# Performance work log

Hardware: AMD Instinct MI355X
Metric: run time of the kernel (lower is better)

## Reference

```python
import jax, jax.numpy as jnp
import numpy as np

N = 10000   # nodes
E = 80000   # edges per graph (avg degree 8)
H = 32      # hidden width (hard-coded in module)
VD0 = 2048  # visual_dim for gcn_0
VD1 = 256   # visual_dim // 8 for gcn_b21


def setup_inputs() -> dict:
    key = jax.random.key(0)
    ks = jax.random.split(key, 16)
    rn = lambda k, s, sc=1.0: jax.random.normal(k, s, dtype=jnp.float32) * sc
    return {
        "x": rn(ks[0], (N, 9)),
        "vis0": rn(ks[1], (N, VD0)),
        "vis1": rn(ks[2], (N, VD1)),
        "edge_index0": jax.random.randint(ks[3], (2, E), 0, N),
        "edge_index1": jax.random.randint(ks[4], (2, E), 0, N),
        # input_mlp: Linear(9,32) -> BatchNorm1d(32) (eval) -> PReLU -> Dropout(0) -> Linear(32,32)
        "W_in1": rn(ks[5], (9, H), 0.3), "b_in1": jnp.zeros((H,), jnp.float32),
        "bn_gamma": jnp.ones((H,), jnp.float32), "bn_beta": jnp.zeros((H,), jnp.float32),
        "bn_mean": jnp.zeros((H,), jnp.float32), "bn_var": jnp.ones((H,), jnp.float32),
        "prelu_a": jnp.asarray(0.25, jnp.float32),
        "W_in2": rn(ks[6], (H, H), 0.15), "b_in2": jnp.zeros((H,), jnp.float32),
        "w_node": rn(ks[7], (H, 1), 0.15), "b_node": jnp.zeros((1,), jnp.float32),
        "W_c0": rn(ks[8], (H, H), 0.15), "b_c0": jnp.zeros((H,), jnp.float32),
        "W_c1": rn(ks[9], (H, H), 0.15), "b_c1": jnp.zeros((H,), jnp.float32),
        "w_p0": rn(ks[10], (H, 1), 0.15), "b_p0": jnp.zeros((1,), jnp.float32),
        "w_p1": rn(ks[11], (H, 1), 0.15), "b_p1": jnp.zeros((1,), jnp.float32),
    }


def _cm_cos_conv(h, edge_index, vis, W, b):
    # gather-weight-scatter: w_e = cos(vis[src], vis[dst]); out_i = (sum_e->i w_e * h[src_e]) @ W + b
    src, dst = edge_index[0], edge_index[1]
    vn = vis * jax.lax.rsqrt(jnp.sum(vis * vis, axis=-1, keepdims=True) + 1e-8)
    w = jnp.sum(vn[src] * vn[dst], axis=-1)  # [E] cosine similarity per edge
    agg = jax.ops.segment_sum(h[src] * w[:, None], dst, num_segments=h.shape[0])  # [N,H]
    return agg @ W + b  # conv_activation=None -> identity


def reference(x, vis0, vis1, edge_index0, edge_index1, W_in1, b_in1, bn_gamma, bn_beta, bn_mean, bn_var, prelu_a, W_in2, b_in2, w_node, b_node, W_c0, b_c0, W_c1, b_c1, w_p0, b_p0, w_p1, b_p1):
    h = x @ W_in1 + b_in1
    h = bn_gamma * (h - bn_mean) * jax.lax.rsqrt(bn_var + 1e-5) + bn_beta
    h = jnp.where(h >= 0, h, prelu_a * h)  # PReLU (single shared slope)
    h = h @ W_in2 + b_in2                   # [N,32] shared for graphs 0 and 4
    nodes_scores = (h @ w_node + b_node)[:, 0]
    h0 = _cm_cos_conv(h, edge_index0, vis0, W_c0, b_c0)
    h1 = _cm_cos_conv(h, edge_index1, vis1, W_c1, b_c1)
    s0 = (h0 @ w_p0 + b_p0)[:, 0]
    s1 = (h1 @ w_p1 + b_p1)[:, 0]
    return nodes_scores + s0 + s1
```

## Files before the change

kernel.cpp:

```cpp
#include <hip/hip_runtime.h>

#define N_NODES 10000
#define NE      80000
#define H       32
#define VD0     2048
#define VD1     256

#define EDGE_CAP 32

#define NODE_BLOCKS  40
#define NC_BLOCKS    2500
#define PREP_BLOCKS  (NODE_BLOCKS + 2 * NC_BLOCKS)

#define EDGE0_PHASES  4
#define EDGE0_GBLK    2500
#define EDGE0_BLOCKS  (EDGE0_PHASES * EDGE0_GBLK)
#define EDGE1_BLOCKS  2500
#define EDGE_BLOCKS   (EDGE0_BLOCKS + EDGE1_BLOCKS)

__device__ inline unsigned short f2bf_rne(float f) {
    unsigned int u = __float_as_uint(f);
    u += 0x7fffu + ((u >> 16) & 1u);
    return (unsigned short)(u >> 16);
}
__device__ inline float bflo(unsigned int u) { return __uint_as_float(u << 16); }
__device__ inline float bfhi(unsigned int u) { return __uint_as_float(u & 0xffff0000u); }
__device__ inline float bfs(unsigned short u) { return __uint_as_float((unsigned int)u << 16); }

__device__ inline float dot8_bf16(uint4 a, uint4 b) {
    float s;
    s  = bflo(a.x) * bflo(b.x) + bfhi(a.x) * bfhi(b.x);
    s += bflo(a.y) * bflo(b.y) + bfhi(a.y) * bfhi(b.y);
    s += bflo(a.z) * bflo(b.z) + bfhi(a.z) * bfhi(b.z);
    s += bflo(a.w) * bflo(b.w) + bfhi(a.w) * bfhi(b.w);
    return s;
}
__device__ inline float dot4_bf16(uint2 a, uint2 b) {
    return bflo(a.x) * bflo(b.x) + bfhi(a.x) * bfhi(b.x)
         + bflo(a.y) * bflo(b.y) + bfhi(a.y) * bfhi(b.y);
}

template <int VD>
__device__ inline void normconv_node(const float* __restrict__ vis,
                                     unsigned short* __restrict__ vn,
                                     int node, int lane)
{
    const float4* v = (const float4*)(vis + (size_t)node * VD);
    float4 f[VD / 256];
    float acc = 0.f;
    #pragma unroll
    for (int it = 0; it < VD / 256; it++) {
        f[it] = v[it * 64 + lane];
        acc += f[it].x * f[it].x + f[it].y * f[it].y + f[it].z * f[it].z + f[it].w * f[it].w;
    }
    #pragma unroll
    for (int o = 32; o; o >>= 1) acc += __shfl_xor(acc, o);
    const float inv = rsqrtf(acc + 1e-8f);
    ushort4* o4 = (ushort4*)(vn + (size_t)node * VD);
    #pragma unroll
    for (int it = 0; it < VD / 256; it++) {
        ushort4 r;
        r.x = f2bf_rne(f[it].x * inv);
        r.y = f2bf_rne(f[it].y * inv);
        r.z = f2bf_rne(f[it].z * inv);
        r.w = f2bf_rne(f[it].w * inv);
        o4[it * 64 + lane] = r;
    }
}

__global__ __launch_bounds__(256) void prep_kernel(
    const float* __restrict__ x,
    const float* __restrict__ vis0, const float* __restrict__ vis1,
    const float* __restrict__ W_in1, const float* __restrict__ b_in1,
    const float* __restrict__ bn_gamma, const float* __restrict__ bn_beta,
    const float* __restrict__ bn_mean, const float* __restrict__ bn_var,
    const float* __restrict__ prelu_a,
    const float* __restrict__ W_in2, const float* __restrict__ b_in2,
    const float* __restrict__ w_node, const float* __restrict__ b_node,
    const float* __restrict__ W_c0, const float* __restrict__ b_c0,
    const float* __restrict__ W_c1, const float* __restrict__ b_c1,
    const float* __restrict__ w_p0, const float* __restrict__ b_p0,
    const float* __restrict__ w_p1, const float* __restrict__ b_p1,
    float* __restrict__ out, float* __restrict__ p0w, float* __restrict__ p1w,
    unsigned short* __restrict__ vn0, unsigned short* __restrict__ vn1)
{
    const int bid = blockIdx.x;
    const int t   = threadIdx.x;

    if (bid < NODE_BLOCKS) {
        __shared__ float sW1[9 * H];
        __shared__ float sW2[H * H];
        __shared__ float sU0[H], sU1[H], sWn[H];
        __shared__ float sB1[H], sB2[H], sSc[H], sSh[H];
        __shared__ float sC;

        for (int i = t; i < 9 * H; i += 256) sW1[i] = W_in1[i];
        for (int i = t; i < H * H; i += 256) sW2[i] = W_in2[i];
        if (t < H) {
            sB1[t] = b_in1[t];
            sB2[t] = b_in2[t];
            float sc = bn_gamma[t] * rsqrtf(bn_var[t] + 1e-5f);
            sSc[t] = sc;
            sSh[t] = bn_beta[t] - bn_mean[t] * sc;
            sWn[t] = w_node[t];
            float u0 = 0.f, u1 = 0.f;
            for (int j = 0; j < H; j++) {
                u0 += W_c0[t * H + j] * w_p0[j];
                u1 += W_c1[t * H + j] * w_p1[j];
            }
            sU0[t] = u0; sU1[t] = u1;
        }
        if (t == 0) {
            float c0 = b_p0[0], c1 = b_p1[0];
            for (int j = 0; j < H; j++) { c0 += b_c0[j] * w_p0[j]; c1 += b_c1[j] * w_p1[j]; }
            sC = c0 + c1 + b_node[0];
        }
        __syncthreads();

        const float a = prelu_a[0];
        const int n = bid * 256 + t;
        if (n >= N_NODES) return;

        float xi[9];
        #pragma unroll
        for (int i = 0; i < 9; i++) xi[i] = x[n * 9 + i];

        float tt[H];
        #pragma unroll
        for (int j = 0; j < H; j++) {
            float s = sB1[j];
            #pragma unroll
            for (int i = 0; i < 9; i++) s += xi[i] * sW1[i * H + j];
            s = s * sSc[j] + sSh[j];
            tt[j] = s >= 0.f ? s : a * s;
        }

        float ns = 0.f, p0 = 0.f, p1 = 0.f;
        #pragma unroll
        for (int k = 0; k < H; k++) {
            float h = sB2[k];
            #pragma unroll
            for (int j = 0; j < H; j++) h += tt[j] * sW2[j * H + k];
            ns += h * sWn[k];
            p0 += h * sU0[k];
            p1 += h * sU1[k];
        }
        out[n] = ns + sC;
        p0w[n] = p0;
        p1w[n] = p1;
    } else if (bid < NODE_BLOCKS + NC_BLOCKS) {
        const int node = ((bid - NODE_BLOCKS) * 256 + t) >> 6;
        if (node < N_NODES) normconv_node<VD0>(vis0, vn0, node, t & 63);
    } else {
        const int node = ((bid - NODE_BLOCKS - NC_BLOCKS) * 256 + t) >> 6;
        if (node < N_NODES) normconv_node<VD1>(vis1, vn1, node, t & 63);
    }
}

__global__ __launch_bounds__(256) void scatter_kernel(
    const int* __restrict__ ei0, int* __restrict__ cur0, uint2* __restrict__ b0,
    const float* __restrict__ p0w, const unsigned short* __restrict__ vn0,
    const int* __restrict__ ei1, int* __restrict__ cur1, uint2* __restrict__ b1,
    const float* __restrict__ p1w, const unsigned short* __restrict__ vn1,
    float* __restrict__ out)
{
    const int e = blockIdx.x * 256 + threadIdx.x;
    if (e >= NE) return;
    {
        const int s = ei0[e];
        const int d = ei0[NE + e];
        const int pos = atomicAdd(&cur0[d], 1);
        if (pos < EDGE_CAP) {
            b0[d * EDGE_CAP + pos] = make_uint2((unsigned)(s * (VD0 * 2)),
                                                __float_as_uint(p0w[s]));
        } else {
            const unsigned short* a = vn0 + (size_t)s * VD0;
            const unsigned short* c = vn0 + (size_t)d * VD0;
            float acc = 0.f;
            for (int i = 0; i < VD0; i++) acc += bfs(a[i]) * bfs(c[i]);
            atomicAdd(&out[d], acc * p0w[s]);
        }
    }
    {
        const int s = ei1[e];
        const int d = ei1[NE + e];
        const int pos = atomicAdd(&cur1[d], 1);
        if (pos < EDGE_CAP) {
            b1[d * EDGE_CAP + pos] = make_uint2((unsigned)(s * (VD1 * 2)),
                                                __float_as_uint(p1w[s]));
        } else {
            const unsigned short* a = vn1 + (size_t)s * VD1;
            const unsigned short* c = vn1 + (size_t)d * VD1;
            float acc = 0.f;
            for (int i = 0; i < VD1; i++) acc += bfs(a[i]) * bfs(c[i]);
            atomicAdd(&out[d], acc * p1w[s]);
        }
    }
}

__global__ __launch_bounds__(256) void edge_kernel_fused(
    const unsigned short* __restrict__ vn0,
    const uint2* __restrict__ b0, const int* __restrict__ cur0,
    const unsigned short* __restrict__ vn1,
    const uint2* __restrict__ b1, const int* __restrict__ cur1,
    float* __restrict__ out)
{
    const int bid  = blockIdx.x;
    const int lane = threadIdx.x & 63;

    if (bid < EDGE0_BLOCKS) {
        const int phase = bid / EDGE0_GBLK;
        const int group = bid % EDGE0_GBLK;
        const int d     = group * 4 + (threadIdx.x >> 6);
        int cnt = cur0[d];
        if (cnt <= 0) return;
        cnt = cnt < EDGE_CAP ? cnt : EDGE_CAP;
        const int last = cnt - 1;

        const char* base = (const char*)vn0;
        const int koffB  = phase * 1024 + lane * 16;
        const uint4 dreg = *(const uint4*)(base + d * (VD0 * 2) + koffB);
        const uint2* eb  = b0 + d * EDGE_CAP;

        float partial = 0.f;
        for (int j = 0; j < cnt; j += 8) {
            uint2 e[8];
            #pragma unroll
            for (int k = 0; k < 8; k++) {
                int jj = j + k;
                jj = jj > last ? last : jj;
                e[k] = eb[jj];
            }
            uint4 r[8];
            #pragma unroll
            for (int k = 0; k < 8; k++)
                r[k] = *(const uint4*)(base + e[k].x + koffB);
            #pragma unroll
            for (int k = 0; k < 8; k++) {
                const float pw = (j + k <= last) ? __uint_as_float(e[k].y) : 0.f;
                partial += dot8_bf16(dreg, r[k]) * pw;
            }
        }
        #pragma unroll
        for (int o = 32; o; o >>= 1) partial += __shfl_down(partial, o);
        if (lane == 0) atomicAdd(&out[d], partial);
    } else {
        const int d = (bid - EDGE0_BLOCKS) * 4 + (threadIdx.x >> 6);
        int cnt = cur1[d];
        if (cnt <= 0) return;
        cnt = cnt < EDGE_CAP ? cnt : EDGE_CAP;
        const int last = cnt - 1;

        const char* base = (const char*)vn1;
        const int koffB  = lane * 8;
        const uint2 dreg = *(const uint2*)(base + d * (VD1 * 2) + koffB);
        const uint2* eb  = b1 + d * EDGE_CAP;

        float partial = 0.f;
        for (int j = 0; j < cnt; j += 8) {
            uint2 e[8];
            #pragma unroll
            for (int k = 0; k < 8; k++) {
                int jj = j + k;
                jj = jj > last ? last : jj;
                e[k] = eb[jj];
            }
            uint2 r[8];
            #pragma unroll
            for (int k = 0; k < 8; k++)
                r[k] = *(const uint2*)(base + e[k].x + koffB);
            #pragma unroll
            for (int k = 0; k < 8; k++) {
                const float pw = (j + k <= last) ? __uint_as_float(e[k].y) : 0.f;
                partial += dot4_bf16(dreg, r[k]) * pw;
            }
        }
        #pragma unroll
        for (int o = 32; o; o >>= 1) partial += __shfl_down(partial, o);
        if (lane == 0) atomicAdd(&out[d], partial);
    }
}

template <int VD>
__global__ __launch_bounds__(256) void norm_kernel(const float* __restrict__ vis,
                                                   float* __restrict__ inv)
{
    const int wave = (blockIdx.x * 256 + threadIdx.x) >> 6;
    const int lane = threadIdx.x & 63;
    if (wave >= N_NODES) return;
    const float4* v = (const float4*)(vis + (size_t)wave * VD);
    float acc = 0.f;
    #pragma unroll
    for (int it = 0; it < VD / 256; it++) {
        float4 f = v[lane + it * 64];
        acc += f.x * f.x + f.y * f.y + f.z * f.z + f.w * f.w;
    }
    #pragma unroll
    for (int o = 32; o; o >>= 1) acc += __shfl_down(acc, o);
    if (lane == 0) inv[wave] = rsqrtf(acc + 1e-8f);
}

template <int VD>
__global__ __launch_bounds__(256) void edge_kernel(
    const float* __restrict__ vis, const int* __restrict__ ei,
    const float* __restrict__ inv, const float* __restrict__ p,
    float* __restrict__ out)
{
    const int wave = (blockIdx.x * 256 + threadIdx.x) >> 6;
    const int lane = threadIdx.x & 63;
    if (wave >= NE) return;
    const int src = ei[wave];
    const int dst = ei[NE + wave];
    const float4* va = (const float4*)(vis + (size_t)src * VD);
    const float4* vb = (const float4*)(vis + (size_t)dst * VD);
    float acc = 0.f;
    #pragma unroll
    for (int it = 0; it < VD / 256; it++) {
        float4 fa = va[lane + it * 64];
        float4 fb = vb[lane + it * 64];
        acc += fa.x * fb.x + fa.y * fb.y + fa.z * fb.z + fa.w * fb.w;
    }
    #pragma unroll
    for (int o = 32; o; o >>= 1) acc += __shfl_down(acc, o);
    if (lane == 0) {
        float w = acc * inv[src] * inv[dst];
        atomicAdd(&out[dst], w * p[src]);
    }
}

__global__ __launch_bounds__(256) void node_kernel_fb(
    const float* __restrict__ x,
    const float* __restrict__ W_in1, const float* __restrict__ b_in1,
    const float* __restrict__ bn_gamma, const float* __restrict__ bn_beta,
    const float* __restrict__ bn_mean, const float* __restrict__ bn_var,
    const float* __restrict__ prelu_a,
    const float* __restrict__ W_in2, const float* __restrict__ b_in2,
    const float* __restrict__ w_node, const float* __restrict__ b_node,
    const float* __restrict__ W_c0, const float* __restrict__ b_c0,
    const float* __restrict__ W_c1, const float* __restrict__ b_c1,
    const float* __restrict__ w_p0, const float* __restrict__ b_p0,
    const float* __restrict__ w_p1, const float* __restrict__ b_p1,
    float* __restrict__ out, float* __restrict__ p0w, float* __restrict__ p1w)
{
    __shared__ float sW1[9 * H];
    __shared__ float sW2[H * H];
    __shared__ float sU0[H], sU1[H], sWn[H];
    __shared__ float sB1[H], sB2[H], sSc[H], sSh[H];
    __shared__ float sC;

    const int t = threadIdx.x;
    for (int i = t; i < 9 * H; i += 256) sW1[i] = W_in1[i];
    for (int i = t; i < H * H; i += 256) sW2[i] = W_in2[i];
    if (t < H) {
        sB1[t] = b_in1[t];
        sB2[t] = b_in2[t];
        float sc = bn_gamma[t] * rsqrtf(bn_var[t] + 1e-5f);
        sSc[t] = sc;
        sSh[t] = bn_beta[t] - bn_mean[t] * sc;
        sWn[t] = w_node[t];
        float u0 = 0.f, u1 = 0.f;
        for (int j = 0; j < H; j++) {
            u0 += W_c0[t * H + j] * w_p0[j];
            u1 += W_c1[t * H + j] * w_p1[j];
        }
        sU0[t] = u0; sU1[t] = u1;
    }
    if (t == 0) {
        float c0 = b_p0[0], c1 = b_p1[0];
        for (int j = 0; j < H; j++) { c0 += b_c0[j] * w_p0[j]; c1 += b_c1[j] * w_p1[j]; }
        sC = c0 + c1 + b_node[0];
    }
    __syncthreads();

    const float a = prelu_a[0];
    const int n = blockIdx.x * 256 + t;
    if (n >= N_NODES) return;

    float xi[9];
    #pragma unroll
    for (int i = 0; i < 9; i++) xi[i] = x[n * 9 + i];

    float tt[H];
    #pragma unroll
    for (int j = 0; j < H; j++) {
        float s = sB1[j];
        #pragma unroll
        for (int i = 0; i < 9; i++) s += xi[i] * sW1[i * H + j];
        s = s * sSc[j] + sSh[j];
        tt[j] = s >= 0.f ? s : a * s;
    }

    float ns = 0.f, p0 = 0.f, p1 = 0.f;
    #pragma unroll
    for (int k = 0; k < H; k++) {
        float h = sB2[k];
        #pragma unroll
        for (int j = 0; j < H; j++) h += tt[j] * sW2[j * H + k];
        ns += h * sWn[k];
        p0 += h * sU0[k];
        p1 += h * sU1[k];
    }
    out[n] = ns + sC;
    p0w[n] = p0;
    p1w[n] = p1;
}

extern "C" void kernel_launch(void* const* d_in, const int* in_sizes, int n_in,
                              void* d_out, int out_size, void* d_ws, size_t ws_size,
                              hipStream_t stream)
{
    const float* x        = (const float*)d_in[0];
    const float* vis0     = (const float*)d_in[1];
    const float* vis1     = (const float*)d_in[2];
    const int*   ei0      = (const int*)d_in[3];
    const int*   ei1      = (const int*)d_in[4];
    const float* W_in1    = (const float*)d_in[5];
    const float* b_in1    = (const float*)d_in[6];
    const float* bn_gamma = (const float*)d_in[7];
    const float* bn_beta  = (const float*)d_in[8];
    const float* bn_mean  = (const float*)d_in[9];
    const float* bn_var   = (const float*)d_in[10];
    const float* prelu_a  = (const float*)d_in[11];
    const float* W_in2    = (const float*)d_in[12];
    const float* b_in2    = (const float*)d_in[13];
    const float* w_node   = (const float*)d_in[14];
    const float* b_node   = (const float*)d_in[15];
    const float* W_c0     = (const float*)d_in[16];
    const float* b_c0     = (const float*)d_in[17];
    const float* W_c1     = (const float*)d_in[18];
    const float* b_c1     = (const float*)d_in[19];
    const float* w_p0     = (const float*)d_in[20];
    const float* b_p0     = (const float*)d_in[21];
    const float* w_p1     = (const float*)d_in[22];
    const float* b_p1     = (const float*)d_in[23];

    float* out = (float*)d_out;

    char* ws = (char*)d_ws;
    float* p0w  = (float*)ws;                  ws += N_NODES * 4;
    float* p1w  = (float*)ws;                  ws += N_NODES * 4;
    float* inv0 = (float*)ws;                  ws += N_NODES * 4;
    float* inv1 = (float*)ws;                  ws += N_NODES * 4;
    unsigned short* vn0 = (unsigned short*)ws; ws += (size_t)N_NODES * VD0 * 2;
    unsigned short* vn1 = (unsigned short*)ws; ws += (size_t)N_NODES * VD1 * 2;
    uint2* b0   = (uint2*)ws;                  ws += (size_t)N_NODES * EDGE_CAP * 8;
    uint2* b1   = (uint2*)ws;                  ws += (size_t)N_NODES * EDGE_CAP * 8;
    int* cur0   = (int*)ws;                    ws += N_NODES * 4;
    int* cur1   = (int*)ws;                    ws += N_NODES * 4;
    const size_t need = (size_t)(ws - (char*)d_ws);

    if (ws_size >= need) {
        hipMemsetAsync(cur0, 0, 2 * N_NODES * sizeof(int), stream);

        prep_kernel<<<PREP_BLOCKS, 256, 0, stream>>>(
            x, vis0, vis1,
            W_in1, b_in1, bn_gamma, bn_beta, bn_mean, bn_var, prelu_a,
            W_in2, b_in2, w_node, b_node, W_c0, b_c0, W_c1, b_c1,
            w_p0, b_p0, w_p1, b_p1,
            out, p0w, p1w, vn0, vn1);

        scatter_kernel<<<(NE + 255) / 256, 256, 0, stream>>>(
            ei0, cur0, b0, p0w, vn0,
            ei1, cur1, b1, p1w, vn1, out);

        edge_kernel_fused<<<EDGE_BLOCKS, 256, 0, stream>>>(
            vn0, b0, cur0, vn1, b1, cur1, out);
    } else {
        node_kernel_fb<<<(N_NODES + 255) / 256, 256, 0, stream>>>(
            x, W_in1, b_in1, bn_gamma, bn_beta, bn_mean, bn_var, prelu_a,
            W_in2, b_in2, w_node, b_node, W_c0, b_c0, W_c1, b_c1,
            w_p0, b_p0, w_p1, b_p1, out, p0w, p1w);
        norm_kernel<VD0><<<(N_NODES * 64 + 255) / 256, 256, 0, stream>>>(vis0, inv0);
        norm_kernel<VD1><<<(N_NODES * 64 + 255) / 256, 256, 0, stream>>>(vis1, inv1);
        edge_kernel<VD0><<<(NE * 64 + 255) / 256, 256, 0, stream>>>(vis0, ei0, inv0, p0w, out);
        edge_kernel<VD1><<<(NE * 64 + 255) / 256, 256, 0, stream>>>(vis1, ei1, inv1, p1w, out);
    }
}
```

Before: 238.8 us.

## Fuse prep, scatter and edge stages into one cooperative persistent kernel

Replaces the memset plus three separate kernel launches with a single cooperative persistent kernel. It zeroes the counters in-kernel, then runs the node MLP and normalisation stage, the edge bucketing stage and the per-destination dot stage, separated by grid-wide syncs. The goal is to remove launch gaps and kernel tails. The graph-0 edge stage also splits into 8 phases of 4 bf16 elements instead of 4 phases of 8, which changes per-lane load width and parallelism. Grid syncs and a grid capped at 4096 blocks with forced occupancy of 4 may leave stages under-parallelised, and the per-call static occupancy query adds host logic.

```diff
diff --git a/kernel.cpp b/kernel.cpp
--- a/kernel.cpp
+++ b/kernel.cpp
@@ -1,4 +1,7 @@
 #include <hip/hip_runtime.h>
+#include <hip/hip_cooperative_groups.h>
+
+namespace cg = cooperative_groups;
 
 #define N_NODES 10000
 #define NE      80000
@@ -8,15 +11,15 @@
 
 #define EDGE_CAP 32
 
-#define NODE_BLOCKS  40
-#define NC_BLOCKS    2500
-#define PREP_BLOCKS  (NODE_BLOCKS + 2 * NC_BLOCKS)
-
-#define EDGE0_PHASES  4
-#define EDGE0_GBLK    2500
-#define EDGE0_BLOCKS  (EDGE0_PHASES * EDGE0_GBLK)
-#define EDGE1_BLOCKS  2500
-#define EDGE_BLOCKS   (EDGE0_BLOCKS + EDGE1_BLOCKS)
+#define A_MLP    40
+#define A_NC0    2500
+#define A_NC1    2500
+#define A_UNITS  (A_MLP + A_NC0 + A_NC1)
+#define ZERO_BLOCKS 79
+
+#define C_PHASES 8
+#define C_G0     (C_PHASES * 2500)
+#define C_UNITS  (C_G0 + 2500)
 
 __device__ inline unsigned short f2bf_rne(float f) {
     unsigned int u = __float_as_uint(f);
@@ -27,18 +30,30 @@
 __device__ inline float bfhi(unsigned int u) { return __uint_as_float(u & 0xffff0000u); }
 __device__ inline float bfs(unsigned short u) { return __uint_as_float((unsigned int)u << 16); }
 
-__device__ inline float dot8_bf16(uint4 a, uint4 b) {
-    float s;
-    s  = bflo(a.x) * bflo(b.x) + bfhi(a.x) * bfhi(b.x);
-    s += bflo(a.y) * bflo(b.y) + bfhi(a.y) * bfhi(b.y);
-    s += bflo(a.z) * bflo(b.z) + bfhi(a.z) * bfhi(b.z);
-    s += bflo(a.w) * bflo(b.w) + bfhi(a.w) * bfhi(b.w);
-    return s;
-}
 __device__ inline float dot4_bf16(uint2 a, uint2 b) {
     return bflo(a.x) * bflo(b.x) + bfhi(a.x) * bfhi(b.x)
          + bflo(a.y) * bflo(b.y) + bfhi(a.y) * bfhi(b.y);
 }
+
+struct KP {
+    const float* x;
+    const float* vis0; const float* vis1;
+    const int* ei0; const int* ei1;
+    const float* W_in1; const float* b_in1;
+    const float* bn_gamma; const float* bn_beta;
+    const float* bn_mean; const float* bn_var;
+    const float* prelu_a;
+    const float* W_in2; const float* b_in2;
+    const float* w_node; const float* b_node;
+    const float* W_c0; const float* b_c0;
+    const float* W_c1; const float* b_c1;
+    const float* w_p0; const float* b_p0;
+    const float* w_p1; const float* b_p1;
+    float* out; float* p0w; float* p1w;
+    unsigned short* vn0; unsigned short* vn1;
+    uint2* b0; uint2* b1;
+    int* cur0; int* cur1;
+};
 
 template <int VD>
 __device__ inline void normconv_node(const float* __restrict__ vis,
@@ -68,159 +83,130 @@
     }
 }
 
-__global__ __launch_bounds__(256) void prep_kernel(
-    const float* __restrict__ x,
-    const float* __restrict__ vis0, const float* __restrict__ vis1,
-    const float* __restrict__ W_in1, const float* __restrict__ b_in1,
-    const float* __restrict__ bn_gamma, const float* __restrict__ bn_beta,
-    const float* __restrict__ bn_mean, const float* __restrict__ bn_var,
-    const float* __restrict__ prelu_a,
-    const float* __restrict__ W_in2, const float* __restrict__ b_in2,
-    const float* __restrict__ w_node, const float* __restrict__ b_node,
-    const float* __restrict__ W_c0, const float* __restrict__ b_c0,
-    const float* __restrict__ W_c1, const float* __restrict__ b_c1,
-    const float* __restrict__ w_p0, const float* __restrict__ b_p0,
-    const float* __restrict__ w_p1, const float* __restrict__ b_p1,
-    float* __restrict__ out, float* __restrict__ p0w, float* __restrict__ p1w,
-    unsigned short* __restrict__ vn0, unsigned short* __restrict__ vn1)
-{
-    const int bid = blockIdx.x;
-    const int t   = threadIdx.x;
-
-    if (bid < NODE_BLOCKS) {
+__device__ inline void stageA_unit(const KP& p, int u, int t)
+{
+    if (u < A_MLP) {
         __shared__ float sW1[9 * H];
         __shared__ float sW2[H * H];
         __shared__ float sU0[H], sU1[H], sWn[H];
         __shared__ float sB1[H], sB2[H], sSc[H], sSh[H];
         __shared__ float sC;
 
-        for (int i = t; i < 9 * H; i += 256) sW1[i] = W_in1[i];
-        for (int i = t; i < H * H; i += 256) sW2[i] = W_in2[i];
+        for (int i = t; i < 9 * H; i += 256) sW1[i] = p.W_in1[i];
+        for (int i = t; i < H * H; i += 256) sW2[i] = p.W_in2[i];
         if (t < H) {
-            sB1[t] = b_in1[t];
-            sB2[t] = b_in2[t];
-            float sc = bn_gamma[t] * rsqrtf(bn_var[t] + 1e-5f);
+            sB1[t] = p.b_in1[t];
+            sB2[t] = p.b_in2[t];
+            float sc = p.bn_gamma[t] * rsqrtf(p.bn_var[t] + 1e-5f);
             sSc[t] = sc;
-            sSh[t] = bn_beta[t] - bn_mean[t] * sc;
-            sWn[t] = w_node[t];
+            sSh[t] = p.bn_beta[t] - p.bn_mean[t] * sc;
+            sWn[t] = p.w_node[t];
             float u0 = 0.f, u1 = 0.f;
             for (int j = 0; j < H; j++) {
-                u0 += W_c0[t * H + j] * w_p0[j];
-                u1 += W_c1[t * H + j] * w_p1[j];
+                u0 += p.W_c0[t * H + j] * p.w_p0[j];
+                u1 += p.W_c1[t * H + j] * p.w_p1[j];
             }
             sU0[t] = u0; sU1[t] = u1;
         }
         if (t == 0) {
-            float c0 = b_p0[0], c1 = b_p1[0];
-            for (int j = 0; j < H; j++) { c0 += b_c0[j] * w_p0[j]; c1 += b_c1[j] * w_p1[j]; }
-            sC = c0 + c1 + b_node[0];
+            float c0 = p.b_p0[0], c1 = p.b_p1[0];
+            for (int j = 0; j < H; j++) { c0 += p.b_c0[j] * p.w_p0[j]; c1 += p.b_c1[j] * p.w_p1[j]; }
+            sC = c0 + c1 + p.b_node[0];
         }
         __syncthreads();
 
-        const float a = prelu_a[0];
-        const int n = bid * 256 + t;
-        if (n >= N_NODES) return;
-
-        float xi[9];
-        #pragma unroll
-        for (int i = 0; i < 9; i++) xi[i] = x[n * 9 + i];
-
-        float tt[H];
-        #pragma unroll
-        for (int j = 0; j < H; j++) {
-            float s = sB1[j];
-            #pragma unroll
-            for (int i = 0; i < 9; i++) s += xi[i] * sW1[i * H + j];
-            s = s * sSc[j] + sSh[j];
-            tt[j] = s >= 0.f ? s : a * s;
-        }
-
-        float ns = 0.f, p0 = 0.f, p1 = 0.f;
-        #pragma unroll
-        for (int k = 0; k < H; k++) {
-            float h = sB2[k];
-            #pragma unroll
-            for (int j = 0; j < H; j++) h += tt[j] * sW2[j * H + k];
-            ns += h * sWn[k];
-            p0 += h * sU0[k];
-            p1 += h * sU1[k];
-        }
-        out[n] = ns + sC;
-        p0w[n] = p0;
-        p1w[n] = p1;
-    } else if (bid < NODE_BLOCKS + NC_BLOCKS) {
-        const int node = ((bid - NODE_BLOCKS) * 256 + t) >> 6;
-        if (node < N_NODES) normconv_node<VD0>(vis0, vn0, node, t & 63);
+        const float a = p.prelu_a[0];
+        const int n = u * 256 + t;
+        if (n < N_NODES) {
+            float xi[9];
+            #pragma unroll
+            for (int i = 0; i < 9; i++) xi[i] = p.x[n * 9 + i];
+
+            float tt[H];
+            #pragma unroll
+            for (int j = 0; j < H; j++) {
+                float s = sB1[j];
+                #pragma unroll
+                for (int i = 0; i < 9; i++) s += xi[i] * sW1[i * H + j];
+                s = s * sSc[j] + sSh[j];
+                tt[j] = s >= 0.f ? s : a * s;
+            }
+
+            float ns = 0.f, p0 = 0.f, p1 = 0.f;
+            #pragma unroll
+            for (int k = 0; k < H; k++) {
+                float h = sB2[k];
+                #pragma unroll
+                for (int j = 0; j < H; j++) h += tt[j] * sW2[j * H + k];
+                ns += h * sWn[k];
+                p0 += h * sU0[k];
+                p1 += h * sU1[k];
+            }
+            p.out[n] = ns + sC;
+            p.p0w[n] = p0;
+            p.p1w[n] = p1;
+        }
+        __syncthreads();
+    } else if (u < A_MLP + A_NC0) {
+        const int node = (u - A_MLP) * 4 + (t >> 6);
+        normconv_node<VD0>(p.vis0, p.vn0, node, t & 63);
     } else {
-        const int node = ((bid - NODE_BLOCKS - NC_BLOCKS) * 256 + t) >> 6;
-        if (node < N_NODES) normconv_node<VD1>(vis1, vn1, node, t & 63);
-    }
-}
-
-__global__ __launch_bounds__(256) void scatter_kernel(
-    const int* __restrict__ ei0, int* __restrict__ cur0, uint2* __restrict__ b0,
-    const float* __restrict__ p0w, const unsigned short* __restrict__ vn0,
-    const int* __restrict__ ei1, int* __restrict__ cur1, uint2* __restrict__ b1,
-    const float* __restrict__ p1w, const unsigned short* __restrict__ vn1,
-    float* __restrict__ out)
-{
-    const int e = blockIdx.x * 256 + threadIdx.x;
-    if (e >= NE) return;
+        const int node = (u - A_MLP - A_NC0) * 4 + (t >> 6);
+        normconv_node<VD1>(p.vis1, p.vn1, node, t & 63);
+    }
+}
+
+__device__ inline void stageB_edge(const KP& p, int e)
+{
     {
-        const int s = ei0[e];
-        const int d = ei0[NE + e];
-        const int pos = atomicAdd(&cur0[d], 1);
+        const int s = p.ei0[e];
+        const int d = p.ei0[NE + e];
+        const int pos = atomicAdd(&p.cur0[d], 1);
         if (pos < EDGE_CAP) {
-            b0[d * EDGE_CAP + pos] = make_uint2((unsigned)(s * (VD0 * 2)),
-                                                __float_as_uint(p0w[s]));
+            p.b0[d * EDGE_CAP + pos] = make_uint2((unsigned)(s * (VD0 * 2)),
+                                                  __float_as_uint(p.p0w[s]));
         } else {
-            const unsigned short* a = vn0 + (size_t)s * VD0;
-            const unsigned short* c = vn0 + (size_t)d * VD0;
+            const unsigned short* a = p.vn0 + (size_t)s * VD0;
+            const unsigned short* c = p.vn0 + (size_t)d * VD0;
             float acc = 0.f;
             for (int i = 0; i < VD0; i++) acc += bfs(a[i]) * bfs(c[i]);
-            atomicAdd(&out[d], acc * p0w[s]);
+            atomicAdd(&p.out[d], acc * p.p0w[s]);
         }
     }
     {
-        const int s = ei1[e];
-        const int d = ei1[NE + e];
-        const int pos = atomicAdd(&cur1[d], 1);
+        const int s = p.ei1[e];
+        const int d = p.ei1[NE + e];
+        const int pos = atomicAdd(&p.cur1[d], 1);
         if (pos < EDGE_CAP) {
-            b1[d * EDGE_CAP + pos] = make_uint2((unsigned)(s * (VD1 * 2)),
-                                                __float_as_uint(p1w[s]));
+            p.b1[d * EDGE_CAP + pos] = make_uint2((unsigned)(s * (VD1 * 2)),
+                                                  __float_as_uint(p.p1w[s]));
         } else {
-            const unsigned short* a = vn1 + (size_t)s * VD1;
-            const unsigned short* c = vn1 + (size_t)d * VD1;
+            const unsigned short* a = p.vn1 + (size_t)s * VD1;
+            const unsigned short* c = p.vn1 + (size_t)d * VD1;
             float acc = 0.f;
             for (int i = 0; i < VD1; i++) acc += bfs(a[i]) * bfs(c[i]);
-            atomicAdd(&out[d], acc * p1w[s]);
-        }
-    }
-}
-
-__global__ __launch_bounds__(256) void edge_kernel_fused(
-    const unsigned short* __restrict__ vn0,
-    const uint2* __restrict__ b0, const int* __restrict__ cur0,
-    const unsigned short* __restrict__ vn1,
-    const uint2* __restrict__ b1, const int* __restrict__ cur1,
-    float* __restrict__ out)
-{
-    const int bid  = blockIdx.x;
-    const int lane = threadIdx.x & 63;
-
-    if (bid < EDGE0_BLOCKS) {
-        const int phase = bid / EDGE0_GBLK;
-        const int group = bid % EDGE0_GBLK;
-        const int d     = group * 4 + (threadIdx.x >> 6);
-        int cnt = cur0[d];
+            atomicAdd(&p.out[d], acc * p.p1w[s]);
+        }
+    }
+}
+
+__device__ inline void stageC_unit(const KP& p, int u, int t)
+{
+    const int lane = t & 63;
+
+    if (u < C_G0) {
+        const int phase = u & 7;
+        const int group = u >> 3;
+        const int d     = group * 4 + (t >> 6);
+        int cnt = p.cur0[d];
         if (cnt <= 0) return;
         cnt = cnt < EDGE_CAP ? cnt : EDGE_CAP;
         const int last = cnt - 1;
 
-        const char* base = (const char*)vn0;
-        const int koffB  = phase * 1024 + lane * 16;
-        const uint4 dreg = *(const uint4*)(base + d * (VD0 * 2) + koffB);
-        const uint2* eb  = b0 + d * EDGE_CAP;
+        const char* base = (const char*)p.vn0;
+        const int koffB  = phase * 512 + lane * 8;
+        const uint2 dreg = *(const uint2*)(base + d * (VD0 * 2) + koffB);
+        const uint2* eb  = p.b0 + d * EDGE_CAP;
 
         float partial = 0.f;
         for (int j = 0; j < cnt; j += 8) {
@@ -231,30 +217,30 @@
                 jj = jj > last ? last : jj;
                 e[k] = eb[jj];
             }
-            uint4 r[8];
+            uint2 r[8];
             #pragma unroll
             for (int k = 0; k < 8; k++)
-                r[k] = *(const uint4*)(base + e[k].x + koffB);
+                r[k] = *(const uint2*)(base + e[k].x + koffB);
             #pragma unroll
             for (int k = 0; k < 8; k++) {
                 const float pw = (j + k <= last) ? __uint_as_float(e[k].y) : 0.f;
-                partial += dot8_bf16(dreg, r[k]) * pw;
+                partial += dot4_bf16(dreg, r[k]) * pw;
             }
         }
         #pragma unroll
         for (int o = 32; o; o >>= 1) partial += __shfl_down(partial, o);
-        if (lane == 0) atomicAdd(&out[d], partial);
+        if (lane == 0) atomicAdd(&p.out[d], partial);
     } else {
-        const int d = (bid - EDGE0_BLOCKS) * 4 + (threadIdx.x >> 6);
-        int cnt = cur1[d];
+        const int d = (u - C_G0) * 4 + (t >> 6);
+        int cnt = p.cur1[d];
         if (cnt <= 0) return;
         cnt = cnt < EDGE_CAP ? cnt : EDGE_CAP;
         const int last = cnt - 1;
 
-        const char* base = (const char*)vn1;
+        const char* base = (const char*)p.vn1;
         const int koffB  = lane * 8;
         const uint2 dreg = *(const uint2*)(base + d * (VD1 * 2) + koffB);
-        const uint2* eb  = b1 + d * EDGE_CAP;
+        const uint2* eb  = p.b1 + d * EDGE_CAP;
 
         float partial = 0.f;
         for (int j = 0; j < cnt; j += 8) {
@@ -277,8 +263,42 @@
         }
         #pragma unroll
         for (int o = 32; o; o >>= 1) partial += __shfl_down(partial, o);
-        if (lane == 0) atomicAdd(&out[d], partial);
-    }
+        if (lane == 0) atomicAdd(&p.out[d], partial);
+    }
+}
+
+__global__ __launch_bounds__(256, 4) void mega_kernel(KP p)
+{
+    const int t = threadIdx.x;
+    const int b = blockIdx.x;
+    const int G = gridDim.x;
+
+    for (int i = b * 256 + t; i < 2 * N_NODES; i += G * 256) p.cur0[i] = 0;
+    for (int u = b; u < A_UNITS; u += G) stageA_unit(p, u, t);
+    cg::this_grid().sync();
+    for (int e = b * 256 + t; e < NE; e += G * 256) stageB_edge(p, e);
+    cg::this_grid().sync();
+    for (int u = b; u < C_UNITS; u += G) stageC_unit(p, u, t);
+}
+
+__global__ __launch_bounds__(256) void prep2_kernel(KP p)
+{
+    const int b = blockIdx.x, t = threadIdx.x;
+    if (b < ZERO_BLOCKS) {
+        const int i = b * 256 + t;
+        if (i < 2 * N_NODES) p.cur0[i] = 0;
+    } else {
+        stageA_unit(p, b - ZERO_BLOCKS, t);
+    }
+}
+__global__ __launch_bounds__(256) void scatter2_kernel(KP p)
+{
+    const int e = blockIdx.x * 256 + threadIdx.x;
+    if (e < NE) stageB_edge(p, e);
+}
+__global__ __launch_bounds__(256) void edge2_kernel(KP p)
+{
+    stageC_unit(p, blockIdx.x, threadIdx.x);
 }
 
 template <int VD>
@@ -303,7 +323,7 @@
 template <int VD>
 __global__ __launch_bounds__(256) void edge_kernel(
     const float* __restrict__ vis, const int* __restrict__ ei,
-    const float* __restrict__ inv, const float* __restrict__ p,
+    const float* __restrict__ inv, const float* __restrict__ pz,
     float* __restrict__ out)
 {
     const int wave = (blockIdx.x * 256 + threadIdx.x) >> 6;
@@ -324,155 +344,98 @@
     for (int o = 32; o; o >>= 1) acc += __shfl_down(acc, o);
     if (lane == 0) {
         float w = acc * inv[src] * inv[dst];
-        atomicAdd(&out[dst], w * p[src]);
-    }
-}
-
-__global__ __launch_bounds__(256) void node_kernel_fb(
-    const float* __restrict__ x,
-    const float* __restrict__ W_in1, const float* __restrict__ b_in1,
-    const float* __restrict__ bn_gamma, const float* __restrict__ bn_beta,
-    const float* __restrict__ bn_mean, const float* __restrict__ bn_var,
-    const float* __restrict__ prelu_a,
-    const float* __restrict__ W_in2, const float* __restrict__ b_in2,
-    const float* __restrict__ w_node, const float* __restrict__ b_node,
-    const float* __restrict__ W_c0, const float* __restrict__ b_c0,
-    const float* __restrict__ W_c1, const float* __restrict__ b_c1,
-    const float* __restrict__ w_p0, const float* __restrict__ b_p0,
-    const float* __restrict__ w_p1, const float* __restrict__ b_p1,
-    float* __restrict__ out, float* __restrict__ p0w, float* __restrict__ p1w)
-{
-    __shared__ float sW1[9 * H];
-    __shared__ float sW2[H * H];
-    __shared__ float sU0[H], sU1[H], sWn[H];
-    __shared__ float sB1[H], sB2[H], sSc[H], sSh[H];
-    __shared__ float sC;
-
-    const int t = threadIdx.x;
-    for (int i = t; i < 9 * H; i += 256) sW1[i] = W_in1[i];
-    for (int i = t; i < H * H; i += 256) sW2[i] = W_in2[i];
-    if (t < H) {
-        sB1[t] = b_in1[t];
-        sB2[t] = b_in2[t];
-        float sc = bn_gamma[t] * rsqrtf(bn_var[t] + 1e-5f);
-        sSc[t] = sc;
-        sSh[t] = bn_beta[t] - bn_mean[t] * sc;
-        sWn[t] = w_node[t];
-        float u0 = 0.f, u1 = 0.f;
-        for (int j = 0; j < H; j++) {
-            u0 += W_c0[t * H + j] * w_p0[j];
-            u1 += W_c1[t * H + j] * w_p1[j];
-        }
-        sU0[t] = u0; sU1[t] = u1;
-    }
-    if (t == 0) {
-        float c0 = b_p0[0], c1 = b_p1[0];
-        for (int j = 0; j < H; j++) { c0 += b_c0[j] * w_p0[j]; c1 += b_c1[j] * w_p1[j]; }
-        sC = c0 + c1 + b_node[0];
-    }
-    __syncthreads();
-
-    const float a = prelu_a[0];
-    const int n = blockIdx.x * 256 + t;
-    if (n >= N_NODES) return;
-
-    float xi[9];
-    #pragma unroll
-    for (int i = 0; i < 9; i++) xi[i] = x[n * 9 + i];
-
-    float tt[H];
-    #pragma unroll
-    for (int j = 0; j < H; j++) {
-        float s = sB1[j];
-        #pragma unroll
-        for (int i = 0; i < 9; i++) s += xi[i] * sW1[i * H + j];
-        s = s * sSc[j] + sSh[j];
-        tt[j] = s >= 0.f ? s : a * s;
-    }
-
-    float ns = 0.f, p0 = 0.f, p1 = 0.f;
-    #pragma unroll
-    for (int k = 0; k < H; k++) {
-        float h = sB2[k];
-        #pragma unroll
-        for (int j = 0; j < H; j++) h += tt[j] * sW2[j * H + k];
-        ns += h * sWn[k];
-        p0 += h * sU0[k];
-        p1 += h * sU1[k];
-    }
-    out[n] = ns + sC;
-    p0w[n] = p0;
-    p1w[n] = p1;
+        atomicAdd(&out[dst], w * pz[src]);
+    }
+}
+
+__global__ __launch_bounds__(256) void node_kernel_fb(KP p)
+{
+    stageA_unit(p, (int)blockIdx.x, (int)threadIdx.x);
 }
 
 extern "C" void kernel_launch(void* const* d_in, const int* in_sizes, int n_in,
                               void* d_out, int out_size, void* d_ws, size_t ws_size,
                               hipStream_t stream)
 {
-    const float* x        = (const float*)d_in[0];
-    const float* vis0     = (const float*)d_in[1];
-    const float* vis1     = (const float*)d_in[2];
-    const int*   ei0      = (const int*)d_in[3];
-    const int*   ei1      = (const int*)d_in[4];
-    const float* W_in1    = (const float*)d_in[5];
-    const float* b_in1    = (const float*)d_in[6];
-    const float* bn_gamma = (const float*)d_in[7];
-    const float* bn_beta  = (const float*)d_in[8];
-    const float* bn_mean  = (const float*)d_in[9];
-    const float* bn_var   = (const float*)d_in[10];
-    const float* prelu_a  = (const float*)d_in[11];
-    const float* W_in2    = (const float*)d_in[12];
-    const float* b_in2    = (const float*)d_in[13];
-    const float* w_node   = (const float*)d_in[14];
-    const float* b_node   = (const float*)d_in[15];
-    const float* W_c0     = (const float*)d_in[16];
-    const float* b_c0     = (const float*)d_in[17];
-    const float* W_c1     = (const float*)d_in[18];
-    const float* b_c1     = (const float*)d_in[19];
-    const float* w_p0     = (const float*)d_in[20];
-    const float* b_p0     = (const float*)d_in[21];
-    const float* w_p1     = (const float*)d_in[22];
-    const float* b_p1     = (const float*)d_in[23];
-
-    float* out = (float*)d_out;
+    KP hp;
+    hp.x        = (const float*)d_in[0];
+    hp.vis0     = (const float*)d_in[1];
+    hp.vis1     = (const float*)d_in[2];
+    hp.ei0      = (const int*)d_in[3];
+    hp.ei1      = (const int*)d_in[4];
+    hp.W_in1    = (const float*)d_in[5];
+    hp.b_in1    = (const float*)d_in[6];
+    hp.bn_gamma = (const float*)d_in[7];
+    hp.bn_beta  = (const float*)d_in[8];
+    hp.bn_mean  = (const float*)d_in[9];
+    hp.bn_var   = (const float*)d_in[10];
+    hp.prelu_a  = (const float*)d_in[11];
+    hp.W_in2    = (const float*)d_in[12];
+    hp.b_in2    = (const float*)d_in[13];
+    hp.w_node   = (const float*)d_in[14];
+    hp.b_node   = (const float*)d_in[15];
+    hp.W_c0     = (const float*)d_in[16];
+    hp.b_c0     = (const float*)d_in[17];
+    hp.W_c1     = (const float*)d_in[18];
+    hp.b_c1     = (const float*)d_in[19];
+    hp.w_p0     = (const float*)d_in[20];
+    hp.b_p0     = (const float*)d_in[21];
+    hp.w_p1     = (const float*)d_in[22];
+    hp.b_p1     = (const float*)d_in[23];
+    hp.out      = (float*)d_out;
 
     char* ws = (char*)d_ws;
-    float* p0w  = (float*)ws;                  ws += N_NODES * 4;
-    float* p1w  = (float*)ws;                  ws += N_NODES * 4;
-    float* inv0 = (float*)ws;                  ws += N_NODES * 4;
-    float* inv1 = (float*)ws;                  ws += N_NODES * 4;
-    unsigned short* vn0 = (unsigned short*)ws; ws += (size_t)N_NODES * VD0 * 2;
-    unsigned short* vn1 = (unsigned short*)ws; ws += (size_t)N_NODES * VD1 * 2;
-    uint2* b0   = (uint2*)ws;                  ws += (size_t)N_NODES * EDGE_CAP * 8;
-    uint2* b1   = (uint2*)ws;                  ws += (size_t)N_NODES * EDGE_CAP * 8;
-    int* cur0   = (int*)ws;                    ws += N_NODES * 4;
-    int* cur1   = (int*)ws;                    ws += N_NODES * 4;
+    hp.p0w  = (float*)ws;                  ws += N_NODES * 4;
+    hp.p1w  = (float*)ws;                  ws += N_NODES * 4;
+    float* inv0 = (float*)ws;              ws += N_NODES * 4;
+    float* inv1 = (float*)ws;              ws += N_NODES * 4;
+    hp.vn0  = (unsigned short*)ws;         ws += (size_t)N_NODES * VD0 * 2;
+    hp.vn1  = (unsigned short*)ws;         ws += (size_t)N_NODES * VD1 * 2;
+    hp.b0   = (uint2*)ws;                  ws += (size_t)N_NODES * EDGE_CAP * 8;
+    hp.b1   = (uint2*)ws;                  ws += (size_t)N_NODES * EDGE_CAP * 8;
+    hp.cur0 = (int*)ws;                    ws += N_NODES * 4;
+    hp.cur1 = (int*)ws;                    ws += N_NODES * 4;
     const size_t need = (size_t)(ws - (char*)d_ws);
 
     if (ws_size >= need) {
-        hipMemsetAsync(cur0, 0, 2 * N_NODES * sizeof(int), stream);
-
-        prep_kernel<<<PREP_BLOCKS, 256, 0, stream>>>(
-            x, vis0, vis1,
-            W_in1, b_in1, bn_gamma, bn_beta, bn_mean, bn_var, prelu_a,
-            W_in2, b_in2, w_node, b_node, W_c0, b_c0, W_c1, b_c1,
-            w_p0, b_p0, w_p1, b_p1,
-            out, p0w, p1w, vn0, vn1);
-
-        scatter_kernel<<<(NE + 255) / 256, 256, 0, stream>>>(
-            ei0, cur0, b0, p0w, vn0,
-            ei1, cur1, b1, p1w, vn1, out);
-
-        edge_kernel_fused<<<EDGE_BLOCKS, 256, 0, stream>>>(
-            vn0, b0, cur0, vn1, b1, cur1, out);
+        static int coop = -2;
+        if (coop == -2) {
+            int nb = 0;
+            if (hipOccupancyMaxActiveBlocksPerMultiprocessor(&nb, mega_kernel, 256, 0)
+                    == hipSuccess && nb > 0)
+                coop = nb;
+            else
+                coop = -1;
+        }
+
+        bool done = false;
+        if (coop > 0) {
+            int G = coop * 256;
+            if (G > 4096) G = 4096;
+            G &= ~7;
+            if (G >= 64) {
+                void* args[] = { (void*)&hp };
+                if (hipLaunchCooperativeKernel((void*)mega_kernel, dim3(G),
+                                               dim3(256), args, 0, stream)
+                        == hipSuccess) {
+                    done = true;
+                } else {
+                    coop = -1;
+                }
+            } else {
+                coop = -1;
+            }
+        }
+        if (!done) {
+            prep2_kernel<<<ZERO_BLOCKS + A_UNITS, 256, 0, stream>>>(hp);
+            scatter2_kernel<<<(NE + 255) / 256, 256, 0, stream>>>(hp);
+            edge2_kernel<<<C_UNITS, 256, 0, stream>>>(hp);
+        }
     } else {
-        node_kernel_fb<<<(N_NODES + 255) / 256, 256, 0, stream>>>(
-            x, W_in1, b_in1, bn_gamma, bn_beta, bn_mean, bn_var, prelu_a,
-            W_in2, b_in2, w_node, b_node, W_c0, b_c0, W_c1, b_c1,
-            w_p0, b_p0, w_p1, b_p1, out, p0w, p1w);
-        norm_kernel<VD0><<<(N_NODES * 64 + 255) / 256, 256, 0, stream>>>(vis0, inv0);
-        norm_kernel<VD1><<<(N_NODES * 64 + 255) / 256, 256, 0, stream>>>(vis1, inv1);
-        edge_kernel<VD0><<<(NE * 64 + 255) / 256, 256, 0, stream>>>(vis0, ei0, inv0, p0w, out);
-        edge_kernel<VD1><<<(NE * 64 + 255) / 256, 256, 0, stream>>>(vis1, ei1, inv1, p1w, out);
-    }
-}
+        node_kernel_fb<<<A_MLP, 256, 0, stream>>>(hp);
+        norm_kernel<VD0><<<(N_NODES * 64 + 255) / 256, 256, 0, stream>>>(hp.vis0, inv0);
+        norm_kernel<VD1><<<(N_NODES * 64 + 255) / 256, 256, 0, stream>>>(hp.vis1, inv1);
+        edge_kernel<VD0><<<(NE * 64 + 255) / 256, 256, 0, stream>>>(hp.vis0, hp.ei0, inv0, hp.p0w, hp.out);
+        edge_kernel<VD1><<<(NE * 64 + 255) / 256, 256, 0, stream>>>(hp.vis1, hp.ei1, inv1, hp.p1w, hp.out);
+    }
+}
```

New measurement: 472.1 us. 1.98x slower.
